# Kernel tuning notes

Measured on AMD Instinct MI355X. Metric: run time of the kernel, lower is better.

Reference implementation:

```python
import jax, jax.numpy as jnp
import numpy as np

NUM_GRAPHS = 128
NODES_PER_GRAPH = 512
NUM_NODES = NUM_GRAPHS * NODES_PER_GRAPH
NUM_EDGES = NUM_NODES * 16
IN_DIM = 64
HID = 128
NUM_HEADS = 4
BN_EPS = 1e-5


def setup_inputs() -> dict:
    key = jax.random.key(0)
    ks = jax.random.split(key, 12)
    x = jax.random.normal(ks[0], (NUM_NODES, IN_DIM), dtype=jnp.float32)
    edge_index = jax.random.randint(ks[1], (2, NUM_EDGES), 0, NUM_NODES, dtype=jnp.int32)
    batch = jnp.repeat(jnp.arange(NUM_GRAPHS, dtype=jnp.int32), NODES_PER_GRAPH)
    s = 0.05
    W0 = jax.random.normal(ks[2], (IN_DIM, HID), dtype=jnp.float32) * s
    b0 = jnp.zeros((HID,), jnp.float32)
    Wh = jax.random.normal(ks[3], (3, HID, HID), dtype=jnp.float32) * s  # convs 1..3
    bh = jnp.zeros((3, HID), jnp.float32)
    bn_gamma = jnp.ones((4, HID), jnp.float32)
    bn_beta = jnp.zeros((4, HID), jnp.float32)
    bn_mean = jnp.zeros((4, HID), jnp.float32)
    bn_var = jnp.ones((4, HID), jnp.float32)
    attn_in_w = jax.random.normal(ks[4], (3 * HID, HID), dtype=jnp.float32) * s
    attn_in_b = jnp.zeros((3 * HID,), jnp.float32)
    attn_out_w = jax.random.normal(ks[5], (HID, HID), dtype=jnp.float32) * s
    attn_out_b = jnp.zeros((HID,), jnp.float32)
    return dict(x=x, W0=W0, b0=b0, Wh=Wh, bh=bh, bn_gamma=bn_gamma, bn_beta=bn_beta,
                bn_mean=bn_mean, bn_var=bn_var, attn_in_w=attn_in_w, attn_in_b=attn_in_b,
                attn_out_w=attn_out_w, attn_out_b=attn_out_b, edge_index=edge_index, batch=batch)


def _forward(x, W0, b0, Wh, bh, bn_gamma, bn_beta, bn_mean, bn_var,
             attn_in_w, attn_in_b, attn_out_w, attn_out_b, edge_index, batch):
    N = x.shape[0]
    src, dst = edge_index[0], edge_index[1]
    # GCN symmetric normalization with self-loops (PyG GCNConv)
    deg = jax.ops.segment_sum(jnp.ones_like(src, jnp.float32), dst, num_segments=N) + 1.0
    dis = jax.lax.rsqrt(deg)                      # deg^{-1/2}
    enorm = (dis[src] * dis[dst])[:, None]        # per-edge norm
    self_norm = (dis * dis)[:, None]              # self-loop norm

    def gcn(h, W, b):
        h = h @ W
        agg = jax.ops.segment_sum(h[src] * enorm, dst, num_segments=N)
        return agg + h * self_norm + b

    def bn(h, i):
        scale = bn_gamma[i] * jax.lax.rsqrt(bn_var[i] + BN_EPS)
        return (h - bn_mean[i]) * scale + bn_beta[i]  # eval-mode BN

    # dropout is identity in eval mode
    h = jax.nn.relu(bn(gcn(x, W0, b0), 0))
    h = jax.nn.relu(bn(gcn(h, Wh[0], bh[0]), 1))
    h = jax.nn.relu(bn(gcn(h, Wh[1], bh[1]), 2))
    f = jax.nn.relu(bn(gcn(h, Wh[2], bh[2]), 3))   # [N, HID]

    # per-graph self-attention (equal-size contiguous graphs -> batched MHA)
    dh = HID // NUM_HEADS
    xg = f.reshape(NUM_GRAPHS, NODES_PER_GRAPH, HID)
    qkv = xg @ attn_in_w.T + attn_in_b            # [G, n, 3H]
    q, k, v = jnp.split(qkv, 3, axis=-1)

    def heads(t):
        return t.reshape(NUM_GRAPHS, NODES_PER_GRAPH, NUM_HEADS, dh).transpose(0, 2, 1, 3)
    q, k, v = heads(q), heads(k), heads(v)
    scores = jnp.einsum('ghnd,ghmd->ghnm', q, k) / np.sqrt(dh).astype(np.float32)
    attn = jax.nn.softmax(scores, axis=-1)
    o = jnp.einsum('ghnm,ghmd->ghnd', attn, v).transpose(0, 2, 1, 3).reshape(NUM_GRAPHS, NODES_PER_GRAPH, HID)
    o = o @ attn_out_w.T + attn_out_b
    final = o.reshape(N, HID)

    # global mean pool over batch indices
    cnt = jax.ops.segment_sum(jnp.ones((N,), jnp.float32), batch, num_segments=NUM_GRAPHS)
    graph_emb = jax.ops.segment_sum(final, batch, num_segments=NUM_GRAPHS) / cnt[:, None]
    return final, graph_emb


def reference(x, W0, b0, Wh, bh, bn_gamma, bn_beta, bn_mean, bn_var,
              attn_in_w, attn_in_b, attn_out_w, attn_out_b, edge_index, batch):
    return _forward(x, W0, b0, Wh, bh, bn_gamma, bn_beta, bn_mean, bn_var,
                    attn_in_w, attn_in_b, attn_out_w, attn_out_b, edge_index, batch)
```

## Files before the change

### kernel.cpp

```cpp
#include <hip/hip_runtime.h>
#include <hip/hip_bf16.h>
#include <cstdint>
#include <cstddef>

#define N_NODES 65536
#define N_EDGES 1048576
#define N_GRAPHS 128
#define NPG 512
#define IN_DIM 64
#define HID 128
#define BN_EPS 1e-5f

typedef __attribute__((ext_vector_type(8))) short bf16x8;
typedef __attribute__((ext_vector_type(4))) float f32x4;
typedef __attribute__((ext_vector_type(8))) unsigned short u16x8;

__device__ inline unsigned short f2bf(float f) {
  unsigned u = __builtin_bit_cast(unsigned, f);
  u = u + 0x7fffu + ((u >> 16) & 1u);
  return (unsigned short)(u >> 16);
}
__device__ inline float bf2f(unsigned short h) {
  unsigned u = ((unsigned)h) << 16;
  return __builtin_bit_cast(float, u);
}
__device__ inline void split_bf(float v, unsigned short& hi, unsigned short& lo) {
  hi = f2bf(v);
  lo = f2bf(v - bf2f(hi));
}

__global__ __launch_bounds__(256) void hist_kernel(const int* __restrict__ dst,
                                                   int* __restrict__ deg) {
  int e = blockIdx.x * 256 + threadIdx.x;
  if (e < N_EDGES) atomicAdd(&deg[dst[e]], 1);
}

__global__ __launch_bounds__(256) void dis_kernel(const int* __restrict__ deg,
                                                  float* __restrict__ dis) {
  int n = blockIdx.x * 256 + threadIdx.x;
  if (n < N_NODES) dis[n] = 1.0f / sqrtf((float)deg[n] + 1.0f);
}

__global__ __launch_bounds__(1024) void scan_kernel(const int* __restrict__ deg,
                                                    int* __restrict__ offsets,
                                                    int* __restrict__ cursor) {
  __shared__ int sums[1024];
  int t = threadIdx.x;
  int base = t * 64;
  const int4* dp = (const int4*)(deg + base);
  int s = 0;
#pragma unroll
  for (int i = 0; i < 16; i++) {
    int4 v = dp[i];
    s += v.x + v.y + v.z + v.w;
  }
  sums[t] = s;
  __syncthreads();
  for (int off = 1; off < 1024; off <<= 1) {
    int v = (t >= off) ? sums[t - off] : 0;
    __syncthreads();
    sums[t] += v;
    __syncthreads();
  }
  int run = (t == 0) ? 0 : sums[t - 1];
#pragma unroll
  for (int i = 0; i < 16; i++) {
    int4 v = dp[i];
    int idx = base + i * 4;
    offsets[idx] = run; cursor[idx] = run; run += v.x;
    offsets[idx + 1] = run; cursor[idx + 1] = run; run += v.y;
    offsets[idx + 2] = run; cursor[idx + 2] = run; run += v.z;
    offsets[idx + 3] = run; cursor[idx + 3] = run; run += v.w;
  }
  if (t == 1023) offsets[N_NODES] = run;
}

__global__ __launch_bounds__(256) void fill_kernel(const int* __restrict__ src,
                                                   const int* __restrict__ dst,
                                                   int* __restrict__ cursor,
                                                   int* __restrict__ csr) {
  int e = blockIdx.x * 256 + threadIdx.x;
  if (e < N_EDGES) {
    int d = dst[e];
    int slot = atomicAdd(&cursor[d], 1);
    csr[slot] = src[e];
  }
}

__global__ __launch_bounds__(256) void agg64_kernel(const float* __restrict__ x,
                                                    const float* __restrict__ dis,
                                                    const int* __restrict__ offsets,
                                                    const int* __restrict__ csr,
                                                    unsigned short* __restrict__ zhi,
                                                    unsigned short* __restrict__ zlo) {
  int node = blockIdx.x * 4 + (threadIdx.x >> 6);
  int lane = threadIdx.x & 63;
  float dn = dis[node];
  float acc = x[(size_t)node * 64 + lane] * dn * dn;
  int beg = offsets[node], end = offsets[node + 1];
  int k = beg;
  for (; k + 4 <= end; k += 4) {
    int s0 = csr[k], s1 = csr[k + 1], s2 = csr[k + 2], s3 = csr[k + 3];
    float w0 = dn * dis[s0], w1 = dn * dis[s1], w2 = dn * dis[s2], w3 = dn * dis[s3];
    float v0 = x[(size_t)s0 * 64 + lane];
    float v1 = x[(size_t)s1 * 64 + lane];
    float v2 = x[(size_t)s2 * 64 + lane];
    float v3 = x[(size_t)s3 * 64 + lane];
    acc = fmaf(w0, v0, acc);
    acc = fmaf(w1, v1, acc);
    acc = fmaf(w2, v2, acc);
    acc = fmaf(w3, v3, acc);
  }
  for (; k < end; k++) {
    int s = csr[k];
    acc = fmaf(dn * dis[s], x[(size_t)s * 64 + lane], acc);
  }
  unsigned short h_, l_;
  split_bf(acc, h_, l_);
  zhi[(size_t)node * 64 + lane] = h_;
  zlo[(size_t)node * 64 + lane] = l_;
}

__global__ __launch_bounds__(256) void agg128_kernel(const float* __restrict__ h,
                                                     const float* __restrict__ dis,
                                                     const int* __restrict__ offsets,
                                                     const int* __restrict__ csr,
                                                     unsigned short* __restrict__ zhi,
                                                     unsigned short* __restrict__ zlo) {
  int node = blockIdx.x * 4 + (threadIdx.x >> 6);
  int lane = threadIdx.x & 63;
  float dn = dis[node];
  float sn = dn * dn;
  const float* hr = h + (size_t)node * 128;
  float a0 = hr[lane] * sn;
  float a1 = hr[lane + 64] * sn;
  int beg = offsets[node], end = offsets[node + 1];
  int k = beg;
  for (; k + 4 <= end; k += 4) {
    int s0 = csr[k], s1 = csr[k + 1], s2 = csr[k + 2], s3 = csr[k + 3];
    float w0 = dn * dis[s0], w1 = dn * dis[s1], w2 = dn * dis[s2], w3 = dn * dis[s3];
    const float* p0 = h + (size_t)s0 * 128;
    const float* p1 = h + (size_t)s1 * 128;
    const float* p2 = h + (size_t)s2 * 128;
    const float* p3 = h + (size_t)s3 * 128;
    float u0 = p0[lane], d0 = p0[lane + 64];
    float u1 = p1[lane], d1 = p1[lane + 64];
    float u2 = p2[lane], d2 = p2[lane + 64];
    float u3 = p3[lane], d3 = p3[lane + 64];
    a0 = fmaf(w0, u0, a0); a1 = fmaf(w0, d0, a1);
    a0 = fmaf(w1, u1, a0); a1 = fmaf(w1, d1, a1);
    a0 = fmaf(w2, u2, a0); a1 = fmaf(w2, d2, a1);
    a0 = fmaf(w3, u3, a0); a1 = fmaf(w3, d3, a1);
  }
  for (; k < end; k++) {
    int s = csr[k];
    float w = dn * dis[s];
    const float* hs = h + (size_t)s * 128;
    a0 = fmaf(w, hs[lane], a0);
    a1 = fmaf(w, hs[lane + 64], a1);
  }
  unsigned short h0, l0, h1, l1;
  split_bf(a0, h0, l0);
  split_bf(a1, h1, l1);
  zhi[(size_t)node * 128 + lane] = h0;
  zlo[(size_t)node * 128 + lane] = l0;
  zhi[(size_t)node * 128 + lane + 64] = h1;
  zlo[(size_t)node * 128 + lane + 64] = l1;
}

template <bool TRANS>
__global__ __launch_bounds__(256) void wprep_kernel(const float* __restrict__ W, int K, int O,
                                                    unsigned short* __restrict__ hi,
                                                    unsigned short* __restrict__ lo) {
  int idx = blockIdx.x * 256 + threadIdx.x;
  int KC = K / 32;
  int total = (O / 16) * KC * 64;
  if (idx >= total) return;
  int lane = idx & 63;
  int rest = idx >> 6;
  int kc = rest % KC;
  int nt = rest / KC;
  int n = nt * 16 + (lane & 15);
  int kb = kc * 32 + (lane >> 4) * 8;
  unsigned short* hp = hi + (size_t)idx * 8;
  unsigned short* lp = lo + (size_t)idx * 8;
#pragma unroll
  for (int j = 0; j < 8; j++) {
    int k = kb + j;
    float v = TRANS ? W[(size_t)n * K + k] : W[(size_t)k * O + n];
    unsigned short h_, l_;
    split_bf(v, h_, l_);
    hp[j] = h_;
    lp[j] = l_;
  }
}

template <int K, int O, bool DOBN, bool DORELU, bool SPLIT_OUT>
__global__ __launch_bounds__(256) void gemm_mfma(
    const unsigned short* __restrict__ Ahi, const unsigned short* __restrict__ Alo,
    const unsigned short* __restrict__ Whi, const unsigned short* __restrict__ Wlo,
    const float* __restrict__ bias,
    const float* __restrict__ gamma, const float* __restrict__ beta,
    const float* __restrict__ mean, const float* __restrict__ var,
    float* __restrict__ Cf, unsigned short* __restrict__ Chi,
    unsigned short* __restrict__ Clo) {
  constexpr int KC = K / 32;
  int wave = threadIdx.x >> 6;
  int lane = threadIdx.x & 63;
  int m0 = blockIdx.x * 128 + wave * 32;
  int o0 = blockIdx.y * 128;
  int mrow = lane & 15;
  int kseg = (lane >> 4) * 8;

  f32x4 acc[2][8];
#pragma unroll
  for (int mt = 0; mt < 2; mt++)
#pragma unroll
    for (int nt = 0; nt < 8; nt++) acc[mt][nt] = (f32x4)0.0f;

#pragma unroll
  for (int kc = 0; kc < KC; kc++) {
    bf16x8 ah[2], al[2];
#pragma unroll
    for (int mt = 0; mt < 2; mt++) {
      size_t aoff = (size_t)(m0 + mt * 16 + mrow) * K + kc * 32 + kseg;
      ah[mt] = *(const bf16x8*)(Ahi + aoff);
      al[mt] = *(const bf16x8*)(Alo + aoff);
    }
#pragma unroll
    for (int nt = 0; nt < 8; nt++) {
      size_t foff = (((size_t)(blockIdx.y * 8 + nt) * KC + kc) * 64 + lane) * 8;
      bf16x8 bh = *(const bf16x8*)(Whi + foff);
      bf16x8 bl = *(const bf16x8*)(Wlo + foff);
#pragma unroll
      for (int mt = 0; mt < 2; mt++) {
        acc[mt][nt] = __builtin_amdgcn_mfma_f32_16x16x32_bf16(ah[mt], bh, acc[mt][nt], 0, 0, 0);
        acc[mt][nt] = __builtin_amdgcn_mfma_f32_16x16x32_bf16(ah[mt], bl, acc[mt][nt], 0, 0, 0);
        acc[mt][nt] = __builtin_amdgcn_mfma_f32_16x16x32_bf16(al[mt], bh, acc[mt][nt], 0, 0, 0);
        acc[mt][nt] = __builtin_amdgcn_mfma_f32_16x16x32_bf16(al[mt], bl, acc[mt][nt], 0, 0, 0);
      }
    }
  }

  int ccol = lane & 15;
  int crow0 = (lane >> 4) * 4;
#pragma unroll
  for (int nt = 0; nt < 8; nt++) {
    int c = o0 + nt * 16 + ccol;
    float sc, cb;
    float b = bias[c];
    if (DOBN) {
      sc = gamma[c] * rsqrtf(var[c] + BN_EPS);
      cb = (b - mean[c]) * sc + beta[c];
    } else {
      sc = 1.0f;
      cb = b;
    }
#pragma unroll
    for (int mt = 0; mt < 2; mt++) {
#pragma unroll
      for (int r = 0; r < 4; r++) {
        float v = fmaf(acc[mt][nt][r], sc, cb);
        if (DORELU) v = fmaxf(v, 0.0f);
        size_t row = (size_t)(m0 + mt * 16 + crow0 + r);
        if (SPLIT_OUT) {
          unsigned short h_, l_;
          split_bf(v, h_, l_);
          Chi[row * O + c] = h_;
          Clo[row * O + c] = l_;
        } else {
          Cf[row * O + c] = v;
        }
      }
    }
  }
}

__global__ __launch_bounds__(256) void knorm_kernel(const float* __restrict__ qkv,
                                                    float* __restrict__ kmax2) {
  int g = blockIdx.x >> 2;
  int h = blockIdx.x & 3;
  size_t gbase = (size_t)g * NPG;
  float best = 0.0f;
#pragma unroll
  for (int r = 0; r < 2; r++) {
    int j = r * 256 + threadIdx.x;
    const float* kp = &qkv[(gbase + j) * 384 + 128 + h * 32];
    float s = 0.0f;
#pragma unroll
    for (int i = 0; i < 8; i++) {
      float4 v = *(const float4*)(kp + i * 4);
      s = fmaf(v.x, v.x, s);
      s = fmaf(v.y, v.y, s);
      s = fmaf(v.z, v.z, s);
      s = fmaf(v.w, v.w, s);
    }
    best = fmaxf(best, s);
  }
#pragma unroll
  for (int off = 32; off >= 1; off >>= 1)
    best = fmaxf(best, __shfl_xor(best, off, 64));
  __shared__ float red[4];
  int wave = threadIdx.x >> 6;
  if ((threadIdx.x & 63) == 0) red[wave] = best;
  __syncthreads();
  if (threadIdx.x == 0) {
    float m = fmaxf(fmaxf(red[0], red[1]), fmaxf(red[2], red[3]));
    kmax2[blockIdx.x] = m;
  }
}

__global__ __launch_bounds__(256, 2) void attn_mfma_kernel(
    const float* __restrict__ qkv, const float* __restrict__ kmax2,
    unsigned short* __restrict__ ohi, unsigned short* __restrict__ olo) {
  int b = blockIdx.x;
  int g = b >> 3;
  int h = (b >> 1) & 3;
  int half = b & 1;
  int t = threadIdx.x;
  int wave = t >> 6;
  int lane = t & 63;
  int quad = lane >> 4;
  int l15 = lane & 15;
  size_t gbase = (size_t)g * NPG;
  int qb = half * 256 + wave * 64;

  const float cf = 0.17677669529663687f * 1.4426950408889634f;

  __shared__ unsigned short Kh[32][40], Kl[32][40];
  __shared__ unsigned short Vh[33][40], Vl[33][40];
  __shared__ char wbuf[4][10240] __attribute__((aligned(16)));

  unsigned short* Ph = (unsigned short*)wbuf[wave];
  unsigned short* Pl = Ph + 64 * 40;
  float* Ot = (float*)wbuf[wave];

  bf16x8 qh[4], ql[4];
  float qn2p[4];
#pragma unroll
  for (int mt = 0; mt < 4; mt++) {
    const float* qp = &qkv[(gbase + qb + mt * 16 + l15) * 384 + h * 32 + quad * 8];
    float4 f0 = *(const float4*)qp;
    float4 f1 = *(const float4*)(qp + 4);
    float v[8] = {f0.x * cf, f0.y * cf, f0.z * cf, f0.w * cf,
                  f1.x * cf, f1.y * cf, f1.z * cf, f1.w * cf};
    u16x8 hh, ll;
    float s = 0.0f;
#pragma unroll
    for (int j = 0; j < 8; j++) {
      unsigned short hi_, lo_;
      split_bf(v[j], hi_, lo_);
      hh[j] = hi_;
      ll[j] = lo_;
      s = fmaf(v[j], v[j], s);
    }
    qh[mt] = __builtin_bit_cast(bf16x8, hh);
    ql[mt] = __builtin_bit_cast(bf16x8, ll);
    s += __shfl_xor(s, 16);
    s += __shfl_xor(s, 32);
    qn2p[mt] = s;
  }
  if (quad == 0) {
#pragma unroll
    for (int mt = 0; mt < 4; mt++) Ot[mt * 16 + l15] = qn2p[mt];
  }
  float km2 = kmax2[g * 4 + h];
  float Mq[4][4];
#pragma unroll
  for (int mt = 0; mt < 4; mt++)
#pragma unroll
    for (int r = 0; r < 4; r++)
      Mq[mt][r] = sqrtf(Ot[mt * 16 + quad * 4 + r] * km2);

  f32x4 Oa[4][3];
#pragma unroll
  for (int mt = 0; mt < 4; mt++)
#pragma unroll
    for (int nt = 0; nt < 3; nt++) Oa[mt][nt] = (f32x4)0.0f;

  for (int c = 0; c < 16; c++) {
    __syncthreads();
    if (t >= 128) {
      int t2 = t - 128;
      int key = t2 >> 2;
      int ds = (t2 & 3) * 8;
      const float* kp = &qkv[(gbase + (size_t)(c * 32 + key)) * 384 + 128 + h * 32 + ds];
      float4 f0 = *(const float4*)kp;
      float4 f1 = *(const float4*)(kp + 4);
      float v[8] = {f0.x, f0.y, f0.z, f0.w, f1.x, f1.y, f1.z, f1.w};
      u16x8 hh, ll;
#pragma unroll
      for (int j = 0; j < 8; j++) {
        unsigned short hi_, lo_;
        split_bf(v[j], hi_, lo_);
        hh[j] = hi_;
        ll[j] = lo_;
      }
      *(u16x8*)&Kh[key][ds] = hh;
      *(u16x8*)&Kl[key][ds] = ll;
    } else if (t < 64) {
      int keyb = (t & 7) * 4;
      int dvb = (t >> 3) * 4;
      float4 r0 = *(const float4*)&qkv[(gbase + (size_t)(c * 32 + keyb + 0)) * 384 + 256 + h * 32 + dvb];
      float4 r1 = *(const float4*)&qkv[(gbase + (size_t)(c * 32 + keyb + 1)) * 384 + 256 + h * 32 + dvb];
      float4 r2 = *(const float4*)&qkv[(gbase + (size_t)(c * 32 + keyb + 2)) * 384 + 256 + h * 32 + dvb];
      float4 r3 = *(const float4*)&qkv[(gbase + (size_t)(c * 32 + keyb + 3)) * 384 + 256 + h * 32 + dvb];
      float rr[4][4] = {{r0.x, r0.y, r0.z, r0.w}, {r1.x, r1.y, r1.z, r1.w},
                        {r2.x, r2.y, r2.z, r2.w}, {r3.x, r3.y, r3.z, r3.w}};
#pragma unroll
      for (int c2 = 0; c2 < 4; c2++) {
        ushort4 hv, lv;
        unsigned short hi_, lo_;
        split_bf(rr[0][c2], hi_, lo_); hv.x = hi_; lv.x = lo_;
        split_bf(rr[1][c2], hi_, lo_); hv.y = hi_; lv.y = lo_;
        split_bf(rr[2][c2], hi_, lo_); hv.z = hi_; lv.z = lo_;
        split_bf(rr[3][c2], hi_, lo_); hv.w = hi_; lv.w = lo_;
        *(ushort4*)&Vh[dvb + c2][keyb] = hv;
        *(ushort4*)&Vl[dvb + c2][keyb] = lv;
      }
    } else if (t < 68) {
      int i = t - 64;
      u16x8 ones;
#pragma unroll
      for (int j = 0; j < 8; j++) ones[j] = 0x3F80;
      *(u16x8*)&Vh[32][i * 8] = ones;
    }
    __syncthreads();

#pragma unroll
    for (int nt = 0; nt < 2; nt++) {
      bf16x8 bkh = *(const bf16x8*)&Kh[nt * 16 + l15][quad * 8];
      bf16x8 bkl = *(const bf16x8*)&Kl[nt * 16 + l15][quad * 8];
#pragma unroll
      for (int mt = 0; mt < 4; mt++) {
        f32x4 S = (f32x4)0.0f;
        S = __builtin_amdgcn_mfma_f32_16x16x32_bf16(qh[mt], bkh, S, 0, 0, 0);
        S = __builtin_amdgcn_mfma_f32_16x16x32_bf16(qh[mt], bkl, S, 0, 0, 0);
        S = __builtin_amdgcn_mfma_f32_16x16x32_bf16(ql[mt], bkh, S, 0, 0, 0);
        S = __builtin_amdgcn_mfma_f32_16x16x32_bf16(ql[mt], bkl, S, 0, 0, 0);
#pragma unroll
        for (int r = 0; r < 4; r++) {
          float p = __builtin_exp2f(S[r] - Mq[mt][r]);
          unsigned short hi_, lo_;
          split_bf(p, hi_, lo_);
          int row = mt * 16 + quad * 4 + r;
          Ph[row * 40 + nt * 16 + l15] = hi_;
          Pl[row * 40 + nt * 16 + l15] = lo_;
        }
      }
    }
    bf16x8 pah[4], pal[4];
#pragma unroll
    for (int mt = 0; mt < 4; mt++) {
      pah[mt] = *(const bf16x8*)&Ph[(mt * 16 + l15) * 40 + quad * 8];
      pal[mt] = *(const bf16x8*)&Pl[(mt * 16 + l15) * 40 + quad * 8];
    }
#pragma unroll
    for (int nt = 0; nt < 3; nt++) {
      bf16x8 bvh = *(const bf16x8*)&Vh[nt * 16 + l15][quad * 8];
      if (nt < 2) {
        bf16x8 bvl = *(const bf16x8*)&Vl[nt * 16 + l15][quad * 8];
#pragma unroll
        for (int mt = 0; mt < 4; mt++) {
          Oa[mt][nt] = __builtin_amdgcn_mfma_f32_16x16x32_bf16(pah[mt], bvh, Oa[mt][nt], 0, 0, 0);
          Oa[mt][nt] = __builtin_amdgcn_mfma_f32_16x16x32_bf16(pah[mt], bvl, Oa[mt][nt], 0, 0, 0);
          Oa[mt][nt] = __builtin_amdgcn_mfma_f32_16x16x32_bf16(pal[mt], bvh, Oa[mt][nt], 0, 0, 0);
        }
      } else {
#pragma unroll
        for (int mt = 0; mt < 4; mt++) {
          Oa[mt][nt] = __builtin_amdgcn_mfma_f32_16x16x32_bf16(pah[mt], bvh, Oa[mt][nt], 0, 0, 0);
          Oa[mt][nt] = __builtin_amdgcn_mfma_f32_16x16x32_bf16(pal[mt], bvh, Oa[mt][nt], 0, 0, 0);
        }
      }
    }
  }

#pragma unroll
  for (int mt = 0; mt < 4; mt++) {
#pragma unroll
    for (int r = 0; r < 4; r++) {
      int row = mt * 16 + quad * 4 + r;
      Ot[row * 36 + l15] = Oa[mt][0][r];
      Ot[row * 36 + 16 + l15] = Oa[mt][1][r];
      if (l15 == 0) Ot[row * 36 + 32] = Oa[mt][2][r];
    }
  }
  {
    int row = lane;
    float inv = 1.0f / Ot[row * 36 + 32];
    size_t node = gbase + qb + row;
    u16x8 vh, vl;
#pragma unroll
    for (int seg = 0; seg < 4; seg++) {
#pragma unroll
      for (int j = 0; j < 8; j++) {
        unsigned short hi_, lo_;
        split_bf(Ot[row * 36 + seg * 8 + j] * inv, hi_, lo_);
        vh[j] = hi_;
        vl[j] = lo_;
      }
      *(u16x8*)(ohi + node * 128 + h * 32 + seg * 8) = vh;
      *(u16x8*)(olo + node * 128 + h * 32 + seg * 8) = vl;
    }
  }
}

__global__ __launch_bounds__(128) void pool_kernel(const float* __restrict__ fin,
                                                   float* __restrict__ emb) {
  int g = blockIdx.x, c = threadIdx.x;
  const float* p = fin + (size_t)g * NPG * HID + c;
  float s = 0.0f;
  for (int i = 0; i < NPG; i++) s += p[(size_t)i * HID];
  emb[g * HID + c] = s * (1.0f / NPG);
}

extern "C" void kernel_launch(void* const* d_in, const int* in_sizes, int n_in,
                              void* d_out, int out_size, void* d_ws, size_t ws_size,
                              hipStream_t stream) {
  (void)in_sizes; (void)n_in; (void)out_size; (void)ws_size;
  const float* x          = (const float*)d_in[0];
  const float* W0         = (const float*)d_in[1];
  const float* b0         = (const float*)d_in[2];
  const float* Wh         = (const float*)d_in[3];
  const float* bh         = (const float*)d_in[4];
  const float* bn_gamma   = (const float*)d_in[5];
  const float* bn_beta    = (const float*)d_in[6];
  const float* bn_mean    = (const float*)d_in[7];
  const float* bn_var     = (const float*)d_in[8];
  const float* attn_in_w  = (const float*)d_in[9];
  const float* attn_in_b  = (const float*)d_in[10];
  const float* attn_out_w = (const float*)d_in[11];
  const float* attn_out_b = (const float*)d_in[12];
  const int* edge_index   = (const int*)d_in[13];
  const int* src = edge_index;
  const int* dst = edge_index + N_EDGES;

  char* ws = (char*)d_ws;
  size_t off = 0;
  auto alloc = [&](size_t bytes) -> void* {
    void* p = ws + off;
    off += (bytes + 255) & ~(size_t)255;
    return p;
  };
  int*   deg     = (int*)alloc((size_t)N_NODES * 4);
  int*   offsets = (int*)alloc((size_t)(N_NODES + 1) * 4);
  int*   cursor  = (int*)alloc((size_t)N_NODES * 4);
  int*   csr     = (int*)alloc((size_t)N_EDGES * 4);
  float* dis     = (float*)alloc((size_t)N_NODES * 4);
  float* bufA    = (float*)alloc((size_t)N_NODES * HID * 4);
  unsigned short* zhi = (unsigned short*)alloc((size_t)N_NODES * HID * 2);
  unsigned short* zlo = (unsigned short*)alloc((size_t)N_NODES * HID * 2);
  float* qkvb    = (float*)alloc((size_t)N_NODES * 384 * 4);
  float* kmax2   = (float*)alloc((size_t)N_GRAPHS * 4 * 4);
  unsigned short* w0h = (unsigned short*)alloc(8192 * 2);
  unsigned short* w0l = (unsigned short*)alloc(8192 * 2);
  unsigned short* whh[3], *whl[3];
  for (int i = 0; i < 3; i++) {
    whh[i] = (unsigned short*)alloc(16384 * 2);
    whl[i] = (unsigned short*)alloc(16384 * 2);
  }
  unsigned short* wqh = (unsigned short*)alloc(49152 * 2);
  unsigned short* wql = (unsigned short*)alloc(49152 * 2);
  unsigned short* woh = (unsigned short*)alloc(16384 * 2);
  unsigned short* wol = (unsigned short*)alloc(16384 * 2);

  unsigned short* fhi = (unsigned short*)bufA;
  unsigned short* flo = fhi + (size_t)N_NODES * HID;

  float* fin = (float*)d_out;
  float* emb = fin + (size_t)N_NODES * HID;

  hipMemsetAsync(deg, 0, (size_t)N_NODES * 4, stream);
  hist_kernel<<<N_EDGES / 256, 256, 0, stream>>>(dst, deg);
  dis_kernel<<<N_NODES / 256, 256, 0, stream>>>(deg, dis);
  scan_kernel<<<1, 1024, 0, stream>>>(deg, offsets, cursor);
  fill_kernel<<<N_EDGES / 256, 256, 0, stream>>>(src, dst, cursor, csr);

  wprep_kernel<false><<<4, 256, 0, stream>>>(W0, 64, 128, w0h, w0l);
  for (int i = 0; i < 3; i++)
    wprep_kernel<false><<<8, 256, 0, stream>>>(Wh + (size_t)i * HID * HID, 128, 128,
                                               whh[i], whl[i]);
  wprep_kernel<true><<<24, 256, 0, stream>>>(attn_in_w, 128, 384, wqh, wql);
  wprep_kernel<true><<<8, 256, 0, stream>>>(attn_out_w, 128, 128, woh, wol);

  dim3 ggrid(N_NODES / 128, 1);
  agg64_kernel<<<N_NODES / 4, 256, 0, stream>>>(x, dis, offsets, csr, zhi, zlo);
  gemm_mfma<64, 128, true, true, false><<<ggrid, 256, 0, stream>>>(
      zhi, zlo, w0h, w0l, b0, bn_gamma, bn_beta, bn_mean, bn_var, bufA, nullptr, nullptr);
  for (int L = 0; L < 2; L++) {
    agg128_kernel<<<N_NODES / 4, 256, 0, stream>>>(bufA, dis, offsets, csr, zhi, zlo);
    gemm_mfma<128, 128, true, true, false><<<ggrid, 256, 0, stream>>>(
        zhi, zlo, whh[L], whl[L], bh + (size_t)L * HID,
        bn_gamma + (size_t)(L + 1) * HID, bn_beta + (size_t)(L + 1) * HID,
        bn_mean + (size_t)(L + 1) * HID, bn_var + (size_t)(L + 1) * HID,
        bufA, nullptr, nullptr);
  }
  agg128_kernel<<<N_NODES / 4, 256, 0, stream>>>(bufA, dis, offsets, csr, zhi, zlo);
  gemm_mfma<128, 128, true, true, true><<<ggrid, 256, 0, stream>>>(
      zhi, zlo, whh[2], whl[2], bh + (size_t)2 * HID,
      bn_gamma + (size_t)3 * HID, bn_beta + (size_t)3 * HID,
      bn_mean + (size_t)3 * HID, bn_var + (size_t)3 * HID,
      nullptr, fhi, flo);
  dim3 qgrid(N_NODES / 128, 3);
  gemm_mfma<128, 384, false, false, false><<<qgrid, 256, 0, stream>>>(
      fhi, flo, wqh, wql, attn_in_b, nullptr, nullptr, nullptr, nullptr,
      qkvb, nullptr, nullptr);
  knorm_kernel<<<N_GRAPHS * 4, 256, 0, stream>>>(qkvb, kmax2);
  attn_mfma_kernel<<<N_GRAPHS * 4 * 2, 256, 0, stream>>>(qkvb, kmax2, zhi, zlo);
  gemm_mfma<128, 128, false, false, false><<<ggrid, 256, 0, stream>>>(
      zhi, zlo, woh, wol, attn_out_b, nullptr, nullptr, nullptr, nullptr,
      fin, nullptr, nullptr);
  pool_kernel<<<N_GRAPHS, 128, 0, stream>>>(fin, emb);
}
```

Measured before the change: 838.2 us.

## Split node aggregation across waves, drop lo*lo MFMA terms, repad attention LDS

The aggregation kernels now assign one node per block and split its edge list across four waves, then combine the partial sums through shared memory. The intent is better load balance and more memory-level parallelism for the gather, at the cost of a block barrier and a shared-memory reduction. Separately, the lo*lo correction MFMA is removed from the GEMM and from the attention score computation, trading a small amount of precision for fewer matrix ops. The attention LDS strides change from 40 to 36 and 37, using split 8-byte loads and stores, to shrink shared memory and alter the bank-conflict pattern.

```diff
diff --git a/kernel.cpp b/kernel.cpp
--- a/kernel.cpp
+++ b/kernel.cpp
@@ -14,6 +14,7 @@
 typedef __attribute__((ext_vector_type(8))) short bf16x8;
 typedef __attribute__((ext_vector_type(4))) float f32x4;
 typedef __attribute__((ext_vector_type(8))) unsigned short u16x8;
+typedef __attribute__((ext_vector_type(4))) unsigned short u16x4;
 
 __device__ inline unsigned short f2bf(float f) {
   unsigned u = __builtin_bit_cast(unsigned, f);
@@ -27,6 +28,12 @@
 __device__ inline void split_bf(float v, unsigned short& hi, unsigned short& lo) {
   hi = f2bf(v);
   lo = f2bf(v - bf2f(hi));
+}
+__device__ inline bf16x8 ld_bf8(const unsigned short* p) {
+  u16x4 a = *(const u16x4*)p;
+  u16x4 b = *(const u16x4*)(p + 4);
+  u16x8 r = __builtin_shufflevector(a, b, 0, 1, 2, 3, 4, 5, 6, 7);
+  return __builtin_bit_cast(bf16x8, r);
 }
 
 __global__ __launch_bounds__(256) void hist_kernel(const int* __restrict__ dst,
@@ -93,13 +100,22 @@
                                                     const int* __restrict__ csr,
                                                     unsigned short* __restrict__ zhi,
                                                     unsigned short* __restrict__ zlo) {
-  int node = blockIdx.x * 4 + (threadIdx.x >> 6);
+  int node = blockIdx.x;
+  int w = threadIdx.x >> 6;
   int lane = threadIdx.x & 63;
+  __shared__ float ps[4][64];
   float dn = dis[node];
-  float acc = x[(size_t)node * 64 + lane] * dn * dn;
   int beg = offsets[node], end = offsets[node + 1];
-  int k = beg;
-  for (; k + 4 <= end; k += 4) {
+  float acc = 0.0f;
+  if (w == 0) acc = x[(size_t)node * 64 + lane] * dn * dn;
+  int deg = end - beg;
+  int q = (deg + 3) >> 2;
+  int ks = beg + w * q;
+  int ke = ks + q;
+  if (ke > end) ke = end;
+  if (ks > end) ks = end;
+  int k = ks;
+  for (; k + 4 <= ke; k += 4) {
     int s0 = csr[k], s1 = csr[k + 1], s2 = csr[k + 2], s3 = csr[k + 3];
     float w0 = dn * dis[s0], w1 = dn * dis[s1], w2 = dn * dis[s2], w3 = dn * dis[s3];
     float v0 = x[(size_t)s0 * 64 + lane];
@@ -111,14 +127,20 @@
     acc = fmaf(w2, v2, acc);
     acc = fmaf(w3, v3, acc);
   }
-  for (; k < end; k++) {
+  for (; k < ke; k++) {
     int s = csr[k];
     acc = fmaf(dn * dis[s], x[(size_t)s * 64 + lane], acc);
   }
-  unsigned short h_, l_;
-  split_bf(acc, h_, l_);
-  zhi[(size_t)node * 64 + lane] = h_;
-  zlo[(size_t)node * 64 + lane] = l_;
+  ps[w][lane] = acc;
+  __syncthreads();
+  if (threadIdx.x < 64) {
+    int d = threadIdx.x;
+    float v = (ps[0][d] + ps[1][d]) + (ps[2][d] + ps[3][d]);
+    unsigned short h_, l_;
+    split_bf(v, h_, l_);
+    zhi[(size_t)node * 64 + d] = h_;
+    zlo[(size_t)node * 64 + d] = l_;
+  }
 }
 
 __global__ __launch_bounds__(256) void agg128_kernel(const float* __restrict__ h,
@@ -127,16 +149,27 @@
                                                      const int* __restrict__ csr,
                                                      unsigned short* __restrict__ zhi,
                                                      unsigned short* __restrict__ zlo) {
-  int node = blockIdx.x * 4 + (threadIdx.x >> 6);
+  int node = blockIdx.x;
+  int w = threadIdx.x >> 6;
   int lane = threadIdx.x & 63;
+  __shared__ float ps[4][128];
   float dn = dis[node];
-  float sn = dn * dn;
-  const float* hr = h + (size_t)node * 128;
-  float a0 = hr[lane] * sn;
-  float a1 = hr[lane + 64] * sn;
   int beg = offsets[node], end = offsets[node + 1];
-  int k = beg;
-  for (; k + 4 <= end; k += 4) {
+  float a0 = 0.0f, a1 = 0.0f;
+  if (w == 0) {
+    float sn = dn * dn;
+    const float* hr = h + (size_t)node * 128;
+    a0 = hr[lane] * sn;
+    a1 = hr[lane + 64] * sn;
+  }
+  int deg = end - beg;
+  int q = (deg + 3) >> 2;
+  int ks = beg + w * q;
+  int ke = ks + q;
+  if (ke > end) ke = end;
+  if (ks > end) ks = end;
+  int k = ks;
+  for (; k + 4 <= ke; k += 4) {
     int s0 = csr[k], s1 = csr[k + 1], s2 = csr[k + 2], s3 = csr[k + 3];
     float w0 = dn * dis[s0], w1 = dn * dis[s1], w2 = dn * dis[s2], w3 = dn * dis[s3];
     const float* p0 = h + (size_t)s0 * 128;
@@ -152,20 +185,24 @@
     a0 = fmaf(w2, u2, a0); a1 = fmaf(w2, d2, a1);
     a0 = fmaf(w3, u3, a0); a1 = fmaf(w3, d3, a1);
   }
-  for (; k < end; k++) {
+  for (; k < ke; k++) {
     int s = csr[k];
-    float w = dn * dis[s];
+    float wt = dn * dis[s];
     const float* hs = h + (size_t)s * 128;
-    a0 = fmaf(w, hs[lane], a0);
-    a1 = fmaf(w, hs[lane + 64], a1);
-  }
-  unsigned short h0, l0, h1, l1;
-  split_bf(a0, h0, l0);
-  split_bf(a1, h1, l1);
-  zhi[(size_t)node * 128 + lane] = h0;
-  zlo[(size_t)node * 128 + lane] = l0;
-  zhi[(size_t)node * 128 + lane + 64] = h1;
-  zlo[(size_t)node * 128 + lane + 64] = l1;
+    a0 = fmaf(wt, hs[lane], a0);
+    a1 = fmaf(wt, hs[lane + 64], a1);
+  }
+  ps[w][lane] = a0;
+  ps[w][lane + 64] = a1;
+  __syncthreads();
+  if (threadIdx.x < 128) {
+    int d = threadIdx.x;
+    float v = (ps[0][d] + ps[1][d]) + (ps[2][d] + ps[3][d]);
+    unsigned short h_, l_;
+    split_bf(v, h_, l_);
+    zhi[(size_t)node * 128 + d] = h_;
+    zlo[(size_t)node * 128 + d] = l_;
+  }
 }
 
 template <bool TRANS>
@@ -237,7 +274,6 @@
         acc[mt][nt] = __builtin_amdgcn_mfma_f32_16x16x32_bf16(ah[mt], bh, acc[mt][nt], 0, 0, 0);
         acc[mt][nt] = __builtin_amdgcn_mfma_f32_16x16x32_bf16(ah[mt], bl, acc[mt][nt], 0, 0, 0);
         acc[mt][nt] = __builtin_amdgcn_mfma_f32_16x16x32_bf16(al[mt], bh, acc[mt][nt], 0, 0, 0);
-        acc[mt][nt] = __builtin_amdgcn_mfma_f32_16x16x32_bf16(al[mt], bl, acc[mt][nt], 0, 0, 0);
       }
     }
   }
@@ -327,12 +363,12 @@
 
   const float cf = 0.17677669529663687f * 1.4426950408889634f;
 
-  __shared__ unsigned short Kh[32][40], Kl[32][40];
-  __shared__ unsigned short Vh[33][40], Vl[33][40];
-  __shared__ char wbuf[4][10240] __attribute__((aligned(16)));
+  __shared__ unsigned short Kh[32][36], Kl[32][36];
+  __shared__ unsigned short Vh[33][36], Vl[33][36];
+  __shared__ char wbuf[4][9472] __attribute__((aligned(16)));
 
   unsigned short* Ph = (unsigned short*)wbuf[wave];
-  unsigned short* Pl = Ph + 64 * 40;
+  unsigned short* Pl = Ph + 64 * 36;
   float* Ot = (float*)wbuf[wave];
 
   bf16x8 qh[4], ql[4];
@@ -388,16 +424,19 @@
       float4 f0 = *(const float4*)kp;
       float4 f1 = *(const float4*)(kp + 4);
       float v[8] = {f0.x, f0.y, f0.z, f0.w, f1.x, f1.y, f1.z, f1.w};
-      u16x8 hh, ll;
-#pragma unroll
-      for (int j = 0; j < 8; j++) {
+      u16x4 h0, h1, l0, l1;
+#pragma unroll
+      for (int j = 0; j < 4; j++) {
         unsigned short hi_, lo_;
         split_bf(v[j], hi_, lo_);
-        hh[j] = hi_;
-        ll[j] = lo_;
+        h0[j] = hi_; l0[j] = lo_;
+        split_bf(v[j + 4], hi_, lo_);
+        h1[j] = hi_; l1[j] = lo_;
       }
-      *(u16x8*)&Kh[key][ds] = hh;
-      *(u16x8*)&Kl[key][ds] = ll;
+      *(u16x4*)&Kh[key][ds] = h0;
+      *(u16x4*)&Kh[key][ds + 4] = h1;
+      *(u16x4*)&Kl[key][ds] = l0;
+      *(u16x4*)&Kl[key][ds + 4] = l1;
     } else if (t < 64) {
       int keyb = (t & 7) * 4;
       int dvb = (t >> 3) * 4;
@@ -423,43 +462,43 @@
       u16x8 ones;
 #pragma unroll
       for (int j = 0; j < 8; j++) ones[j] = 0x3F80;
-      *(u16x8*)&Vh[32][i * 8] = ones;
+      *(u16x4*)&Vh[32][i * 8] = __builtin_shufflevector(ones, ones, 0, 1, 2, 3);
+      *(u16x4*)&Vh[32][i * 8 + 4] = __builtin_shufflevector(ones, ones, 4, 5, 6, 7);
     }
     __syncthreads();
 
 #pragma unroll
     for (int nt = 0; nt < 2; nt++) {
-      bf16x8 bkh = *(const bf16x8*)&Kh[nt * 16 + l15][quad * 8];
-      bf16x8 bkl = *(const bf16x8*)&Kl[nt * 16 + l15][quad * 8];
+      bf16x8 bkh = ld_bf8(&Kh[nt * 16 + l15][quad * 8]);
+      bf16x8 bkl = ld_bf8(&Kl[nt * 16 + l15][quad * 8]);
 #pragma unroll
       for (int mt = 0; mt < 4; mt++) {
         f32x4 S = (f32x4)0.0f;
         S = __builtin_amdgcn_mfma_f32_16x16x32_bf16(qh[mt], bkh, S, 0, 0, 0);
         S = __builtin_amdgcn_mfma_f32_16x16x32_bf16(qh[mt], bkl, S, 0, 0, 0);
         S = __builtin_amdgcn_mfma_f32_16x16x32_bf16(ql[mt], bkh, S, 0, 0, 0);
-        S = __builtin_amdgcn_mfma_f32_16x16x32_bf16(ql[mt], bkl, S, 0, 0, 0);
 #pragma unroll
         for (int r = 0; r < 4; r++) {
           float p = __builtin_exp2f(S[r] - Mq[mt][r]);
           unsigned short hi_, lo_;
           split_bf(p, hi_, lo_);
           int row = mt * 16 + quad * 4 + r;
-          Ph[row * 40 + nt * 16 + l15] = hi_;
-          Pl[row * 40 + nt * 16 + l15] = lo_;
+          Ph[row * 36 + nt * 16 + l15] = hi_;
+          Pl[row * 36 + nt * 16 + l15] = lo_;
         }
       }
     }
     bf16x8 pah[4], pal[4];
 #pragma unroll
     for (int mt = 0; mt < 4; mt++) {
-      pah[mt] = *(const bf16x8*)&Ph[(mt * 16 + l15) * 40 + quad * 8];
-      pal[mt] = *(const bf16x8*)&Pl[(mt * 16 + l15) * 40 + quad * 8];
+      pah[mt] = ld_bf8(&Ph[(mt * 16 + l15) * 36 + quad * 8]);
+      pal[mt] = ld_bf8(&Pl[(mt * 16 + l15) * 36 + quad * 8]);
     }
 #pragma unroll
     for (int nt = 0; nt < 3; nt++) {
-      bf16x8 bvh = *(const bf16x8*)&Vh[nt * 16 + l15][quad * 8];
+      bf16x8 bvh = ld_bf8(&Vh[nt * 16 + l15][quad * 8]);
       if (nt < 2) {
-        bf16x8 bvl = *(const bf16x8*)&Vl[nt * 16 + l15][quad * 8];
+        bf16x8 bvl = ld_bf8(&Vl[nt * 16 + l15][quad * 8]);
 #pragma unroll
         for (int mt = 0; mt < 4; mt++) {
           Oa[mt][nt] = __builtin_amdgcn_mfma_f32_16x16x32_bf16(pah[mt], bvh, Oa[mt][nt], 0, 0, 0);
@@ -481,14 +520,14 @@
 #pragma unroll
     for (int r = 0; r < 4; r++) {
       int row = mt * 16 + quad * 4 + r;
-      Ot[row * 36 + l15] = Oa[mt][0][r];
-      Ot[row * 36 + 16 + l15] = Oa[mt][1][r];
-      if (l15 == 0) Ot[row * 36 + 32] = Oa[mt][2][r];
+      Ot[row * 37 + l15] = Oa[mt][0][r];
+      Ot[row * 37 + 16 + l15] = Oa[mt][1][r];
+      if (l15 == 0) Ot[row * 37 + 32] = Oa[mt][2][r];
     }
   }
   {
     int row = lane;
-    float inv = 1.0f / Ot[row * 36 + 32];
+    float inv = 1.0f / Ot[row * 37 + 32];
     size_t node = gbase + qb + row;
     u16x8 vh, vl;
 #pragma unroll
@@ -496,7 +535,7 @@
 #pragma unroll
       for (int j = 0; j < 8; j++) {
         unsigned short hi_, lo_;
-        split_bf(Ot[row * 36 + seg * 8 + j] * inv, hi_, lo_);
+        split_bf(Ot[row * 37 + seg * 8 + j] * inv, hi_, lo_);
         vh[j] = hi_;
         vl[j] = lo_;
       }
@@ -585,18 +624,18 @@
   wprep_kernel<true><<<8, 256, 0, stream>>>(attn_out_w, 128, 128, woh, wol);
 
   dim3 ggrid(N_NODES / 128, 1);
-  agg64_kernel<<<N_NODES / 4, 256, 0, stream>>>(x, dis, offsets, csr, zhi, zlo);
+  agg64_kernel<<<N_NODES, 256, 0, stream>>>(x, dis, offsets, csr, zhi, zlo);
   gemm_mfma<64, 128, true, true, false><<<ggrid, 256, 0, stream>>>(
       zhi, zlo, w0h, w0l, b0, bn_gamma, bn_beta, bn_mean, bn_var, bufA, nullptr, nullptr);
   for (int L = 0; L < 2; L++) {
-    agg128_kernel<<<N_NODES / 4, 256, 0, stream>>>(bufA, dis, offsets, csr, zhi, zlo);
+    agg128_kernel<<<N_NODES, 256, 0, stream>>>(bufA, dis, offsets, csr, zhi, zlo);
     gemm_mfma<128, 128, true, true, false><<<ggrid, 256, 0, stream>>>(
         zhi, zlo, whh[L], whl[L], bh + (size_t)L * HID,
         bn_gamma + (size_t)(L + 1) * HID, bn_beta + (size_t)(L + 1) * HID,
         bn_mean + (size_t)(L + 1) * HID, bn_var + (size_t)(L + 1) * HID,
         bufA, nullptr, nullptr);
   }
-  agg128_kernel<<<N_NODES / 4, 256, 0, stream>>>(bufA, dis, offsets, csr, zhi, zlo);
+  agg128_kernel<<<N_NODES, 256, 0, stream>>>(bufA, dis, offsets, csr, zhi, zlo);
   gemm_mfma<128, 128, true, true, true><<<ggrid, 256, 0, stream>>>(
       zhi, zlo, whh[2], whl[2], bh + (size_t)2 * HID,
       bn_gamma + (size_t)3 * HID, bn_beta + (size_t)3 * HID,
```

Result: slower. 904.8 us (+7.9%).

## Precompute per-edge weights, unroll gathers by 8, drop lo*lo MFMA terms, repad LDS

Applied to the files above, without the earlier changes.

The fill kernel now stores a per-edge normalization weight next to the CSR index. This removes the random dis[src] gathers from all four aggregation passes, which also gain an 8-way unrolled gather loop for more loads in flight. The split-bf16 GEMM and attention score MFMAs drop the lo*lo product term, cutting a quarter of those MFMAs at a small precision cost. Attention LDS tiles are re-padded (stride 36/37) with 4-element loads and stores to reduce bank conflicts and shared memory size. In exchange, an extra 4 MB edge-weight array is written once and read on every aggregation.

```diff
diff --git a/kernel.cpp b/kernel.cpp
--- a/kernel.cpp
+++ b/kernel.cpp
@@ -14,6 +14,7 @@
 typedef __attribute__((ext_vector_type(8))) short bf16x8;
 typedef __attribute__((ext_vector_type(4))) float f32x4;
 typedef __attribute__((ext_vector_type(8))) unsigned short u16x8;
+typedef __attribute__((ext_vector_type(4))) unsigned short u16x4;
 
 __device__ inline unsigned short f2bf(float f) {
   unsigned u = __builtin_bit_cast(unsigned, f);
@@ -27,6 +28,12 @@
 __device__ inline void split_bf(float v, unsigned short& hi, unsigned short& lo) {
   hi = f2bf(v);
   lo = f2bf(v - bf2f(hi));
+}
+__device__ inline bf16x8 ld_bf8(const unsigned short* p) {
+  u16x4 a = *(const u16x4*)p;
+  u16x4 b = *(const u16x4*)(p + 4);
+  u16x8 r = __builtin_shufflevector(a, b, 0, 1, 2, 3, 4, 5, 6, 7);
+  return __builtin_bit_cast(bf16x8, r);
 }
 
 __global__ __launch_bounds__(256) void hist_kernel(const int* __restrict__ dst,
@@ -77,18 +84,23 @@
 
 __global__ __launch_bounds__(256) void fill_kernel(const int* __restrict__ src,
                                                    const int* __restrict__ dst,
+                                                   const float* __restrict__ dis,
                                                    int* __restrict__ cursor,
-                                                   int* __restrict__ csr) {
+                                                   int* __restrict__ csr,
+                                                   float* __restrict__ wedge) {
   int e = blockIdx.x * 256 + threadIdx.x;
   if (e < N_EDGES) {
     int d = dst[e];
+    int s = src[e];
     int slot = atomicAdd(&cursor[d], 1);
-    csr[slot] = src[e];
+    csr[slot] = s;
+    wedge[slot] = dis[s] * dis[d];
   }
 }
 
 __global__ __launch_bounds__(256) void agg64_kernel(const float* __restrict__ x,
                                                     const float* __restrict__ dis,
+                                                    const float* __restrict__ wedge,
                                                     const int* __restrict__ offsets,
                                                     const int* __restrict__ csr,
                                                     unsigned short* __restrict__ zhi,
@@ -99,9 +111,22 @@
   float acc = x[(size_t)node * 64 + lane] * dn * dn;
   int beg = offsets[node], end = offsets[node + 1];
   int k = beg;
+  for (; k + 8 <= end; k += 8) {
+    int s[8];
+    float w[8], v[8];
+#pragma unroll
+    for (int i = 0; i < 8; i++) {
+      s[i] = csr[k + i];
+      w[i] = wedge[k + i];
+    }
+#pragma unroll
+    for (int i = 0; i < 8; i++) v[i] = x[(size_t)s[i] * 64 + lane];
+#pragma unroll
+    for (int i = 0; i < 8; i++) acc = fmaf(w[i], v[i], acc);
+  }
   for (; k + 4 <= end; k += 4) {
     int s0 = csr[k], s1 = csr[k + 1], s2 = csr[k + 2], s3 = csr[k + 3];
-    float w0 = dn * dis[s0], w1 = dn * dis[s1], w2 = dn * dis[s2], w3 = dn * dis[s3];
+    float w0 = wedge[k], w1 = wedge[k + 1], w2 = wedge[k + 2], w3 = wedge[k + 3];
     float v0 = x[(size_t)s0 * 64 + lane];
     float v1 = x[(size_t)s1 * 64 + lane];
     float v2 = x[(size_t)s2 * 64 + lane];
@@ -113,7 +138,7 @@
   }
   for (; k < end; k++) {
     int s = csr[k];
-    acc = fmaf(dn * dis[s], x[(size_t)s * 64 + lane], acc);
+    acc = fmaf(wedge[k], x[(size_t)s * 64 + lane], acc);
   }
   unsigned short h_, l_;
   split_bf(acc, h_, l_);
@@ -123,6 +148,7 @@
 
 __global__ __launch_bounds__(256) void agg128_kernel(const float* __restrict__ h,
                                                      const float* __restrict__ dis,
+                                                     const float* __restrict__ wedge,
                                                      const int* __restrict__ offsets,
                                                      const int* __restrict__ csr,
                                                      unsigned short* __restrict__ zhi,
@@ -136,9 +162,29 @@
   float a1 = hr[lane + 64] * sn;
   int beg = offsets[node], end = offsets[node + 1];
   int k = beg;
+  for (; k + 8 <= end; k += 8) {
+    int s[8];
+    float w[8], u[8], d[8];
+#pragma unroll
+    for (int i = 0; i < 8; i++) {
+      s[i] = csr[k + i];
+      w[i] = wedge[k + i];
+    }
+#pragma unroll
+    for (int i = 0; i < 8; i++) {
+      const float* p = h + (size_t)s[i] * 128;
+      u[i] = p[lane];
+      d[i] = p[lane + 64];
+    }
+#pragma unroll
+    for (int i = 0; i < 8; i++) {
+      a0 = fmaf(w[i], u[i], a0);
+      a1 = fmaf(w[i], d[i], a1);
+    }
+  }
   for (; k + 4 <= end; k += 4) {
     int s0 = csr[k], s1 = csr[k + 1], s2 = csr[k + 2], s3 = csr[k + 3];
-    float w0 = dn * dis[s0], w1 = dn * dis[s1], w2 = dn * dis[s2], w3 = dn * dis[s3];
+    float w0 = wedge[k], w1 = wedge[k + 1], w2 = wedge[k + 2], w3 = wedge[k + 3];
     const float* p0 = h + (size_t)s0 * 128;
     const float* p1 = h + (size_t)s1 * 128;
     const float* p2 = h + (size_t)s2 * 128;
@@ -154,10 +200,10 @@
   }
   for (; k < end; k++) {
     int s = csr[k];
-    float w = dn * dis[s];
+    float wt = wedge[k];
     const float* hs = h + (size_t)s * 128;
-    a0 = fmaf(w, hs[lane], a0);
-    a1 = fmaf(w, hs[lane + 64], a1);
+    a0 = fmaf(wt, hs[lane], a0);
+    a1 = fmaf(wt, hs[lane + 64], a1);
   }
   unsigned short h0, l0, h1, l1;
   split_bf(a0, h0, l0);
@@ -237,7 +283,6 @@
         acc[mt][nt] = __builtin_amdgcn_mfma_f32_16x16x32_bf16(ah[mt], bh, acc[mt][nt], 0, 0, 0);
         acc[mt][nt] = __builtin_amdgcn_mfma_f32_16x16x32_bf16(ah[mt], bl, acc[mt][nt], 0, 0, 0);
         acc[mt][nt] = __builtin_amdgcn_mfma_f32_16x16x32_bf16(al[mt], bh, acc[mt][nt], 0, 0, 0);
-        acc[mt][nt] = __builtin_amdgcn_mfma_f32_16x16x32_bf16(al[mt], bl, acc[mt][nt], 0, 0, 0);
       }
     }
   }
@@ -327,12 +372,12 @@
 
   const float cf = 0.17677669529663687f * 1.4426950408889634f;
 
-  __shared__ unsigned short Kh[32][40], Kl[32][40];
-  __shared__ unsigned short Vh[33][40], Vl[33][40];
-  __shared__ char wbuf[4][10240] __attribute__((aligned(16)));
+  __shared__ unsigned short Kh[32][36], Kl[32][36];
+  __shared__ unsigned short Vh[33][36], Vl[33][36];
+  __shared__ char wbuf[4][9472] __attribute__((aligned(16)));
 
   unsigned short* Ph = (unsigned short*)wbuf[wave];
-  unsigned short* Pl = Ph + 64 * 40;
+  unsigned short* Pl = Ph + 64 * 36;
   float* Ot = (float*)wbuf[wave];
 
   bf16x8 qh[4], ql[4];
@@ -388,16 +433,19 @@
       float4 f0 = *(const float4*)kp;
       float4 f1 = *(const float4*)(kp + 4);
       float v[8] = {f0.x, f0.y, f0.z, f0.w, f1.x, f1.y, f1.z, f1.w};
-      u16x8 hh, ll;
-#pragma unroll
-      for (int j = 0; j < 8; j++) {
+      u16x4 h0, h1, l0, l1;
+#pragma unroll
+      for (int j = 0; j < 4; j++) {
         unsigned short hi_, lo_;
         split_bf(v[j], hi_, lo_);
-        hh[j] = hi_;
-        ll[j] = lo_;
+        h0[j] = hi_; l0[j] = lo_;
+        split_bf(v[j + 4], hi_, lo_);
+        h1[j] = hi_; l1[j] = lo_;
       }
-      *(u16x8*)&Kh[key][ds] = hh;
-      *(u16x8*)&Kl[key][ds] = ll;
+      *(u16x4*)&Kh[key][ds] = h0;
+      *(u16x4*)&Kh[key][ds + 4] = h1;
+      *(u16x4*)&Kl[key][ds] = l0;
+      *(u16x4*)&Kl[key][ds + 4] = l1;
     } else if (t < 64) {
       int keyb = (t & 7) * 4;
       int dvb = (t >> 3) * 4;
@@ -423,43 +471,43 @@
       u16x8 ones;
 #pragma unroll
       for (int j = 0; j < 8; j++) ones[j] = 0x3F80;
-      *(u16x8*)&Vh[32][i * 8] = ones;
+      *(u16x4*)&Vh[32][i * 8] = __builtin_shufflevector(ones, ones, 0, 1, 2, 3);
+      *(u16x4*)&Vh[32][i * 8 + 4] = __builtin_shufflevector(ones, ones, 4, 5, 6, 7);
     }
     __syncthreads();
 
 #pragma unroll
     for (int nt = 0; nt < 2; nt++) {
-      bf16x8 bkh = *(const bf16x8*)&Kh[nt * 16 + l15][quad * 8];
-      bf16x8 bkl = *(const bf16x8*)&Kl[nt * 16 + l15][quad * 8];
+      bf16x8 bkh = ld_bf8(&Kh[nt * 16 + l15][quad * 8]);
+      bf16x8 bkl = ld_bf8(&Kl[nt * 16 + l15][quad * 8]);
 #pragma unroll
       for (int mt = 0; mt < 4; mt++) {
         f32x4 S = (f32x4)0.0f;
         S = __builtin_amdgcn_mfma_f32_16x16x32_bf16(qh[mt], bkh, S, 0, 0, 0);
         S = __builtin_amdgcn_mfma_f32_16x16x32_bf16(qh[mt], bkl, S, 0, 0, 0);
         S = __builtin_amdgcn_mfma_f32_16x16x32_bf16(ql[mt], bkh, S, 0, 0, 0);
-        S = __builtin_amdgcn_mfma_f32_16x16x32_bf16(ql[mt], bkl, S, 0, 0, 0);
 #pragma unroll
         for (int r = 0; r < 4; r++) {
           float p = __builtin_exp2f(S[r] - Mq[mt][r]);
           unsigned short hi_, lo_;
           split_bf(p, hi_, lo_);
           int row = mt * 16 + quad * 4 + r;
-          Ph[row * 40 + nt * 16 + l15] = hi_;
-          Pl[row * 40 + nt * 16 + l15] = lo_;
+          Ph[row * 36 + nt * 16 + l15] = hi_;
+          Pl[row * 36 + nt * 16 + l15] = lo_;
         }
       }
     }
     bf16x8 pah[4], pal[4];
 #pragma unroll
     for (int mt = 0; mt < 4; mt++) {
-      pah[mt] = *(const bf16x8*)&Ph[(mt * 16 + l15) * 40 + quad * 8];
-      pal[mt] = *(const bf16x8*)&Pl[(mt * 16 + l15) * 40 + quad * 8];
+      pah[mt] = ld_bf8(&Ph[(mt * 16 + l15) * 36 + quad * 8]);
+      pal[mt] = ld_bf8(&Pl[(mt * 16 + l15) * 36 + quad * 8]);
     }
 #pragma unroll
     for (int nt = 0; nt < 3; nt++) {
-      bf16x8 bvh = *(const bf16x8*)&Vh[nt * 16 + l15][quad * 8];
+      bf16x8 bvh = ld_bf8(&Vh[nt * 16 + l15][quad * 8]);
       if (nt < 2) {
-        bf16x8 bvl = *(const bf16x8*)&Vl[nt * 16 + l15][quad * 8];
+        bf16x8 bvl = ld_bf8(&Vl[nt * 16 + l15][quad * 8]);
 #pragma unroll
         for (int mt = 0; mt < 4; mt++) {
           Oa[mt][nt] = __builtin_amdgcn_mfma_f32_16x16x32_bf16(pah[mt], bvh, Oa[mt][nt], 0, 0, 0);
@@ -481,14 +529,14 @@
 #pragma unroll
     for (int r = 0; r < 4; r++) {
       int row = mt * 16 + quad * 4 + r;
-      Ot[row * 36 + l15] = Oa[mt][0][r];
-      Ot[row * 36 + 16 + l15] = Oa[mt][1][r];
-      if (l15 == 0) Ot[row * 36 + 32] = Oa[mt][2][r];
+      Ot[row * 37 + l15] = Oa[mt][0][r];
+      Ot[row * 37 + 16 + l15] = Oa[mt][1][r];
+      if (l15 == 0) Ot[row * 37 + 32] = Oa[mt][2][r];
     }
   }
   {
     int row = lane;
-    float inv = 1.0f / Ot[row * 36 + 32];
+    float inv = 1.0f / Ot[row * 37 + 32];
     size_t node = gbase + qb + row;
     u16x8 vh, vl;
 #pragma unroll
@@ -496,7 +544,7 @@
 #pragma unroll
       for (int j = 0; j < 8; j++) {
         unsigned short hi_, lo_;
-        split_bf(Ot[row * 36 + seg * 8 + j] * inv, hi_, lo_);
+        split_bf(Ot[row * 37 + seg * 8 + j] * inv, hi_, lo_);
         vh[j] = hi_;
         vl[j] = lo_;
       }
@@ -547,6 +595,7 @@
   int*   offsets = (int*)alloc((size_t)(N_NODES + 1) * 4);
   int*   cursor  = (int*)alloc((size_t)N_NODES * 4);
   int*   csr     = (int*)alloc((size_t)N_EDGES * 4);
+  float* wedge   = (float*)alloc((size_t)N_EDGES * 4);
   float* dis     = (float*)alloc((size_t)N_NODES * 4);
   float* bufA    = (float*)alloc((size_t)N_NODES * HID * 4);
   unsigned short* zhi = (unsigned short*)alloc((size_t)N_NODES * HID * 2);
@@ -575,7 +624,7 @@
   hist_kernel<<<N_EDGES / 256, 256, 0, stream>>>(dst, deg);
   dis_kernel<<<N_NODES / 256, 256, 0, stream>>>(deg, dis);
   scan_kernel<<<1, 1024, 0, stream>>>(deg, offsets, cursor);
-  fill_kernel<<<N_EDGES / 256, 256, 0, stream>>>(src, dst, cursor, csr);
+  fill_kernel<<<N_EDGES / 256, 256, 0, stream>>>(src, dst, dis, cursor, csr, wedge);
 
   wprep_kernel<false><<<4, 256, 0, stream>>>(W0, 64, 128, w0h, w0l);
   for (int i = 0; i < 3; i++)
@@ -585,18 +634,18 @@
   wprep_kernel<true><<<8, 256, 0, stream>>>(attn_out_w, 128, 128, woh, wol);
 
   dim3 ggrid(N_NODES / 128, 1);
-  agg64_kernel<<<N_NODES / 4, 256, 0, stream>>>(x, dis, offsets, csr, zhi, zlo);
+  agg64_kernel<<<N_NODES / 4, 256, 0, stream>>>(x, dis, wedge, offsets, csr, zhi, zlo);
   gemm_mfma<64, 128, true, true, false><<<ggrid, 256, 0, stream>>>(
       zhi, zlo, w0h, w0l, b0, bn_gamma, bn_beta, bn_mean, bn_var, bufA, nullptr, nullptr);
   for (int L = 0; L < 2; L++) {
-    agg128_kernel<<<N_NODES / 4, 256, 0, stream>>>(bufA, dis, offsets, csr, zhi, zlo);
+    agg128_kernel<<<N_NODES / 4, 256, 0, stream>>>(bufA, dis, wedge, offsets, csr, zhi, zlo);
     gemm_mfma<128, 128, true, true, false><<<ggrid, 256, 0, stream>>>(
         zhi, zlo, whh[L], whl[L], bh + (size_t)L * HID,
         bn_gamma + (size_t)(L + 1) * HID, bn_beta + (size_t)(L + 1) * HID,
         bn_mean + (size_t)(L + 1) * HID, bn_var + (size_t)(L + 1) * HID,
         bufA, nullptr, nullptr);
   }
-  agg128_kernel<<<N_NODES / 4, 256, 0, stream>>>(bufA, dis, offsets, csr, zhi, zlo);
+  agg128_kernel<<<N_NODES / 4, 256, 0, stream>>>(bufA, dis, wedge, offsets, csr, zhi, zlo);
   gemm_mfma<128, 128, true, true, true><<<ggrid, 256, 0, stream>>>(
       zhi, zlo, whh[2], whl[2], bh + (size_t)2 * HID,
       bn_gamma + (size_t)3 * HID, bn_beta + (size_t)3 * HID,
```

New measurement: 841.9 us. Within noise of the previous version (+0.4%).
